# Kernel optimization log

Measured on AMD Instinct MI355X. Metric: run time of the kernel, lower is better.

## Reference

```python
import jax, jax.numpy as jnp
import numpy as np

SEQ_LEN = 1024
STRIDE = 256
FFT_LEN = 1024
B, FRAMES, BINS = 64, 512, FFT_LEN // 2 + 1


def _hann_periodic(n):
    # scipy.signal.get_window('hann', n) with fftbins=True (periodic)
    return 0.5 - 0.5 * jnp.cos(2.0 * jnp.pi * jnp.arange(n, dtype=jnp.float32) / n)


def setup_inputs() -> dict:
    key = jax.random.key(0)
    k1, k2 = jax.random.split(key)
    real = jax.random.normal(k1, (B, FRAMES, BINS), dtype=jnp.float32)
    imag = jax.random.normal(k2, (B, FRAMES, BINS), dtype=jnp.float32)
    return {"real": real, "imag": imag}


def reference(real, imag):
    # Per-frame inverse real FFT: (B, F, BINS) complex -> (B, F, FFT_LEN) real
    spec = jax.lax.complex(real, imag)
    frames = jnp.fft.irfft(spec, n=FFT_LEN, axis=-1).astype(jnp.float32)

    # Hann window, padded (symmetrically) to fft_length, then normalized by the
    # periodic overlap-added squared-window sum (Keras' COLA normalization).
    win = _hann_periodic(SEQ_LEN)
    l_pad = (FFT_LEN - SEQ_LEN) // 2
    r_pad = FFT_LEN - SEQ_LEN - l_pad
    win = jnp.pad(win, (l_pad, r_pad))
    L = SEQ_LEN + l_pad + r_pad  # == FFT_LEN here
    denom = jnp.square(win)
    overlaps = -(-L // STRIDE)  # ceil(L / stride)
    denom = jnp.pad(denom, (0, overlaps * STRIDE - L))
    denom = denom.reshape(overlaps, STRIDE).sum(0)  # periodic sum per phase
    denom = jnp.tile(denom, overlaps)[:L]
    win = jnp.where(denom > 1e-10, win / denom, 0.0)

    frames = frames * win  # (B, F, FFT_LEN)

    # Overlap-add: out[b, f*stride + n] += frames[b, f, n]
    out_len = STRIDE * (FRAMES - 1) + FFT_LEN
    idx = jnp.arange(FRAMES)[:, None] * STRIDE + jnp.arange(FFT_LEN)[None, :]  # (F, FFT_LEN)
    out = jnp.zeros((B, out_len), dtype=frames.dtype).at[:, idx].add(frames)

    # center=True trims fft_length//2 from both ends
    half = FFT_LEN // 2
    return out[:, half:out_len - half]
```

## Files before the change

kernel.cpp:

```cpp
#include <hip/hip_runtime.h>

#define BATCH    64
#define FRAMES   512
#define BINS     513
#define OUT_LEN  130816
#define HOPS_PER_BLOCK 13

__device__ __forceinline__ float2 cadd(float2 a, float2 b){ return make_float2(a.x+b.x, a.y+b.y); }
__device__ __forceinline__ float2 csub(float2 a, float2 b){ return make_float2(a.x-b.x, a.y-b.y); }
__device__ __forceinline__ float2 cmul(float2 a, float2 b){
    return make_float2(a.x*b.x - a.y*b.y, a.x*b.y + a.y*b.x);
}
__device__ __forceinline__ float2 cexp_rev(float t){
    return make_float2(__builtin_amdgcn_cosf(t), __builtin_amdgcn_sinf(t));
}
__device__ __forceinline__ int phys(int i){ return i + (i >> 4); }

__device__ __forceinline__ void bfly8(float2 v[8]) {
    float2 t0 = cadd(v[0], v[4]), t1 = csub(v[0], v[4]);
    float2 t2 = cadd(v[2], v[6]), t3 = csub(v[2], v[6]);
    float2 E0 = cadd(t0, t2), E2 = csub(t0, t2);
    float2 E1 = make_float2(t1.x - t3.y, t1.y + t3.x);
    float2 E3 = make_float2(t1.x + t3.y, t1.y - t3.x);
    float2 u0 = cadd(v[1], v[5]), u1 = csub(v[1], v[5]);
    float2 u2 = cadd(v[3], v[7]), u3 = csub(v[3], v[7]);
    float2 O0 = cadd(u0, u2), O2 = csub(u0, u2);
    float2 O1 = make_float2(u1.x - u3.y, u1.y + u3.x);
    float2 O3 = make_float2(u1.x + u3.y, u1.y - u3.x);
    const float C = 0.70710678118654752440f;
    float2 w1 = make_float2(C*(O1.x - O1.y),  C*(O1.x + O1.y));
    float2 w2 = make_float2(-O2.y, O2.x);
    float2 w3 = make_float2(-C*(O3.x + O3.y), C*(O3.x - O3.y));
    v[0] = cadd(E0, O0); v[4] = csub(E0, O0);
    v[1] = cadd(E1, w1); v[5] = csub(E1, w1);
    v[2] = cadd(E2, w2); v[6] = csub(E2, w2);
    v[3] = cadd(E3, w3); v[7] = csub(E3, w3);
}

__global__ __launch_bounds__(1024, 8) void istft_kernel(
    const float* __restrict__ re_g, const float* __restrict__ im_g,
    float* __restrict__ out)
{
    __shared__ float2 Xbuf[16][544];
    __shared__ __align__(16) float win[1024];

    const int tid  = threadIdx.x;
    const int wave = tid >> 6;
    const int lane = tid & 63;
    const int b    = blockIdx.y;
    const int u0   = blockIdx.x * HOPS_PER_BLOCK;
    const int f    = u0 - 1 + wave;
    const bool valid = (f >= 0) && (f < FRAMES);

    win[tid] = (0.5f - 0.5f * __builtin_amdgcn_cosf((float)tid * (1.0f/1024.0f)))
               * (2.0f / 3.0f / 1024.0f);

    float2* Xb = Xbuf[wave];

    if (valid) {
        const long long off = (long long)(b * FRAMES + f) * BINS;
        const float* re = re_g + off;
        const float* im = im_g + off;

        const float a0 = (float)lane * (1.0f/1024.0f);
        float2 v[8];
        #pragma unroll
        for (int j = 0; j < 8; ++j) {
            int k = lane + 64*j;
            float xar = re[k];
            float xai = (k == 0) ? 0.0f : im[k];
            float xcr = re[512 - k];
            float xci = (k == 0) ? 0.0f : im[512 - k];
            float Sx = xar + xcr, Sy = xai - xci;
            float Dx = xar - xcr, Dy = xai + xci;
            float2 tk = cexp_rev(a0 + (float)j * (1.0f/16.0f));
            v[j].x = Sx - tk.x*Dy - tk.y*Dx;
            v[j].y = Sy + tk.x*Dx - tk.y*Dy;
        }

        bfly8(v);
        {
            const float lt = (float)lane * (1.0f/512.0f);
            int basei = phys(8*lane);
            Xb[basei] = v[0];
            #pragma unroll
            for (int t = 1; t < 8; ++t)
                Xb[basei + t] = cmul(v[t], cexp_rev((float)t * lt));
        }
        {
            #pragma unroll
            for (int r = 0; r < 8; ++r) v[r] = Xb[phys(lane + 64*r)];
            bfly8(v);
            int p = lane >> 3, q = lane & 7;
            const float pf = (float)p * (1.0f/64.0f);
            Xb[phys(q + 64*p)] = v[0];
            #pragma unroll
            for (int t = 1; t < 8; ++t)
                Xb[phys(q + 64*p + 8*t)] = cmul(v[t], cexp_rev((float)t * pf));
        }
        {
            #pragma unroll
            for (int r = 0; r < 8; ++r) v[r] = Xb[phys(lane + 64*r)];
            bfly8(v);
            #pragma unroll
            for (int t = 0; t < 8; ++t) Xb[phys(lane + 64*t)] = v[t];
        }
    }
    __syncthreads();

    const int nU    = min(HOPS_PER_BLOCK, (OUT_LEN/256) - u0);
    const int nPair = nU * 128;
    float2* outp2 = (float2*)(out + (long long)b * OUT_LEN + 256 * u0);
    const float2* win2 = (const float2*)win;
    for (int pi = tid; pi < nPair; pi += 1024) {
        int o0 = pi * 2;
        int r  = o0 & 255;
        int u  = u0 + (o0 >> 8);
        float s0 = 0.0f, s1 = 0.0f;
        #pragma unroll
        for (int qq = 0; qq < 4; ++qq) {
            int ff = u + 2 - qq;
            if (ff >= 0 && ff < FRAMES) {
                int w = ff - u0 + 1;
                int h = (r >> 1) + 128*qq;
                float2 z  = Xbuf[w][phys(h)];
                float2 wn = win2[h & 511];
                s0 = fmaf(z.x, wn.x, s0);
                s1 = fmaf(z.y, wn.y, s1);
            }
        }
        outp2[pi] = make_float2(s0, s1);
    }
}

extern "C" void kernel_launch(void* const* d_in, const int* in_sizes, int n_in,
                              void* d_out, int out_size, void* d_ws, size_t ws_size,
                              hipStream_t stream) {
    const float* real = (const float*)d_in[0];
    const float* imag = (const float*)d_in[1];
    float* out = (float*)d_out;

    dim3 grid((OUT_LEN/256 + HOPS_PER_BLOCK - 1) / HOPS_PER_BLOCK, BATCH);
    dim3 block(1024);
    istft_kernel<<<grid, block, 0, stream>>>(real, imag, out);
}
```

Before: 162.5 us.

## Halve block size, each wave computes two frame FFTs, precompute twiddles

The block shrinks from 1024 to 512 threads, and each wave now runs the FFTs for two frames (A and B) in interleaved fashion, sharing per-lane twiddle factors. Twiddles come from one cexp plus complex multiplies rather than one sin/cos per element, and half the window is derived by symmetry from the same cosine. Invalid frames are zero-filled so the overlap-add loop drops its bounds checks. This raises register pressure from the two interleaved FFTs and lowers the threads available per block in exchange for more ILP and fewer transcendental calls.

```diff
diff --git a/kernel.cpp b/kernel.cpp
--- a/kernel.cpp
+++ b/kernel.cpp
@@ -37,7 +37,7 @@
     v[3] = cadd(E3, w3); v[7] = csub(E3, w3);
 }
 
-__global__ __launch_bounds__(1024, 8) void istft_kernel(
+__global__ __launch_bounds__(512, 4) void istft_kernel(
     const float* __restrict__ re_g, const float* __restrict__ im_g,
     float* __restrict__ out)
 {
@@ -49,61 +49,124 @@
     const int lane = tid & 63;
     const int b    = blockIdx.y;
     const int u0   = blockIdx.x * HOPS_PER_BLOCK;
-    const int f    = u0 - 1 + wave;
-    const bool valid = (f >= 0) && (f < FRAMES);
-
-    win[tid] = (0.5f - 0.5f * __builtin_amdgcn_cosf((float)tid * (1.0f/1024.0f)))
-               * (2.0f / 3.0f / 1024.0f);
-
-    float2* Xb = Xbuf[wave];
-
-    if (valid) {
-        const long long off = (long long)(b * FRAMES + f) * BINS;
-        const float* re = re_g + off;
-        const float* im = im_g + off;
-
-        const float a0 = (float)lane * (1.0f/1024.0f);
-        float2 v[8];
-        #pragma unroll
-        for (int j = 0; j < 8; ++j) {
-            int k = lane + 64*j;
-            float xar = re[k];
-            float xai = (k == 0) ? 0.0f : im[k];
-            float xcr = re[512 - k];
-            float xci = (k == 0) ? 0.0f : im[512 - k];
-            float Sx = xar + xcr, Sy = xai - xci;
-            float Dx = xar - xcr, Dy = xai + xci;
-            float2 tk = cexp_rev(a0 + (float)j * (1.0f/16.0f));
-            v[j].x = Sx - tk.x*Dy - tk.y*Dx;
-            v[j].y = Sy + tk.x*Dx - tk.y*Dy;
-        }
-
-        bfly8(v);
-        {
-            const float lt = (float)lane * (1.0f/512.0f);
-            int basei = phys(8*lane);
-            Xb[basei] = v[0];
-            #pragma unroll
-            for (int t = 1; t < 8; ++t)
-                Xb[basei + t] = cmul(v[t], cexp_rev((float)t * lt));
-        }
-        {
-            #pragma unroll
-            for (int r = 0; r < 8; ++r) v[r] = Xb[phys(lane + 64*r)];
-            bfly8(v);
-            int p = lane >> 3, q = lane & 7;
-            const float pf = (float)p * (1.0f/64.0f);
-            Xb[phys(q + 64*p)] = v[0];
-            #pragma unroll
-            for (int t = 1; t < 8; ++t)
-                Xb[phys(q + 64*p + 8*t)] = cmul(v[t], cexp_rev((float)t * pf));
-        }
-        {
-            #pragma unroll
-            for (int r = 0; r < 8; ++r) v[r] = Xb[phys(lane + 64*r)];
-            bfly8(v);
-            #pragma unroll
-            for (int t = 0; t < 8; ++t) Xb[phys(lane + 64*t)] = v[t];
+    const int fA   = u0 - 1 + wave;
+    const int fB   = fA + 8;
+    const bool vA  = (fA >= 0) && (fA < FRAMES);
+    const bool vB  = (fB < FRAMES);
+
+    {
+        const float K = 2.0f / 3.0f / 1024.0f;
+        float c = __builtin_amdgcn_cosf((float)tid * (1.0f/1024.0f));
+        win[tid]       = (0.5f - 0.5f*c) * K;
+        win[tid + 512] = (0.5f + 0.5f*c) * K;
+    }
+
+    float2* XA = Xbuf[wave];
+    float2* XB = Xbuf[wave + 8];
+
+    float2 tk[8];
+    tk[0] = cexp_rev((float)lane * (1.0f/1024.0f));
+    {
+        const float Cq = 0.70710678118654752440f;
+        const float Ca = 0.92387953251128675613f;
+        const float Cb = 0.38268343236508977173f;
+        const float2 C16[8] = {
+            make_float2(1.0f, 0.0f), make_float2( Ca, Cb), make_float2( Cq, Cq),
+            make_float2( Cb, Ca),    make_float2(0.0f,1.0f), make_float2(-Cb, Ca),
+            make_float2(-Cq, Cq),    make_float2(-Ca, Cb)
+        };
+        #pragma unroll
+        for (int j = 1; j < 8; ++j) tk[j] = cmul(tk[0], C16[j]);
+    }
+
+    float2 va[8], vb[8];
+    {
+        const long long offA = (long long)(b * FRAMES + fA) * BINS;
+        if (vA) {
+            const float* re = re_g + offA;
+            const float* im = im_g + offA;
+            #pragma unroll
+            for (int j = 0; j < 8; ++j) {
+                const int k = lane + 64*j;
+                float xar = re[k];
+                float xai = (k == 0) ? 0.0f : im[k];
+                float xcr = re[512 - k];
+                float xci = (k == 0) ? 0.0f : im[512 - k];
+                float Sx = xar + xcr, Sy = xai - xci;
+                float Dx = xar - xcr, Dy = xai + xci;
+                va[j].x = Sx - tk[j].x*Dy - tk[j].y*Dx;
+                va[j].y = Sy + tk[j].x*Dx - tk[j].y*Dy;
+            }
+        } else {
+            #pragma unroll
+            for (int j = 0; j < 8; ++j) va[j] = make_float2(0.0f, 0.0f);
+        }
+        if (vB) {
+            const float* re = re_g + offA + 8LL * BINS;
+            const float* im = im_g + offA + 8LL * BINS;
+            #pragma unroll
+            for (int j = 0; j < 8; ++j) {
+                const int k = lane + 64*j;
+                float xar = re[k];
+                float xai = (k == 0) ? 0.0f : im[k];
+                float xcr = re[512 - k];
+                float xci = (k == 0) ? 0.0f : im[512 - k];
+                float Sx = xar + xcr, Sy = xai - xci;
+                float Dx = xar - xcr, Dy = xai + xci;
+                vb[j].x = Sx - tk[j].x*Dy - tk[j].y*Dx;
+                vb[j].y = Sy + tk[j].x*Dx - tk[j].y*Dy;
+            }
+        } else {
+            #pragma unroll
+            for (int j = 0; j < 8; ++j) vb[j] = make_float2(0.0f, 0.0f);
+        }
+    }
+
+    bfly8(va); bfly8(vb);
+    {
+        const float2 wl = cexp_rev((float)lane * (1.0f/512.0f));
+        const int basei = phys(8*lane);
+        XA[basei] = va[0];
+        XB[basei] = vb[0];
+        float2 wt = wl;
+        #pragma unroll
+        for (int t = 1; t < 8; ++t) {
+            XA[basei + t] = cmul(va[t], wt);
+            XB[basei + t] = cmul(vb[t], wt);
+            if (t < 7) wt = cmul(wt, wl);
+        }
+    }
+    {
+        #pragma unroll
+        for (int r = 0; r < 8; ++r) {
+            va[r] = XA[phys(lane + 64*r)];
+            vb[r] = XB[phys(lane + 64*r)];
+        }
+        bfly8(va); bfly8(vb);
+        const int p = lane >> 3, q = lane & 7;
+        const float2 wp = cexp_rev((float)p * (1.0f/64.0f));
+        const int b2 = q + 64*p;
+        XA[phys(b2)] = va[0];
+        XB[phys(b2)] = vb[0];
+        float2 wt = wp;
+        #pragma unroll
+        for (int t = 1; t < 8; ++t) {
+            XA[phys(b2 + 8*t)] = cmul(va[t], wt);
+            XB[phys(b2 + 8*t)] = cmul(vb[t], wt);
+            if (t < 7) wt = cmul(wt, wp);
+        }
+    }
+    {
+        #pragma unroll
+        for (int r = 0; r < 8; ++r) {
+            va[r] = XA[phys(lane + 64*r)];
+            vb[r] = XB[phys(lane + 64*r)];
+        }
+        bfly8(va); bfly8(vb);
+        #pragma unroll
+        for (int t = 0; t < 8; ++t) {
+            XA[phys(lane + 64*t)] = va[t];
+            XB[phys(lane + 64*t)] = vb[t];
         }
     }
     __syncthreads();
@@ -112,22 +175,18 @@
     const int nPair = nU * 128;
     float2* outp2 = (float2*)(out + (long long)b * OUT_LEN + 256 * u0);
     const float2* win2 = (const float2*)win;
-    for (int pi = tid; pi < nPair; pi += 1024) {
-        int o0 = pi * 2;
-        int r  = o0 & 255;
-        int u  = u0 + (o0 >> 8);
+    for (int pi = tid; pi < nPair; pi += 512) {
+        const int h0   = pi & 127;
+        const int uoff = pi >> 7;
         float s0 = 0.0f, s1 = 0.0f;
         #pragma unroll
         for (int qq = 0; qq < 4; ++qq) {
-            int ff = u + 2 - qq;
-            if (ff >= 0 && ff < FRAMES) {
-                int w = ff - u0 + 1;
-                int h = (r >> 1) + 128*qq;
-                float2 z  = Xbuf[w][phys(h)];
-                float2 wn = win2[h & 511];
-                s0 = fmaf(z.x, wn.x, s0);
-                s1 = fmaf(z.y, wn.y, s1);
-            }
+            const int w_ = uoff + 3 - qq;
+            const int h  = h0 + 128*qq;
+            float2 z  = Xbuf[w_][phys(h)];
+            float2 wn = win2[h];
+            s0 = fmaf(z.x, wn.x, s0);
+            s1 = fmaf(z.y, wn.y, s1);
         }
         outp2[pi] = make_float2(s0, s1);
     }
@@ -141,6 +200,6 @@
     float* out = (float*)d_out;
 
     dim3 grid((OUT_LEN/256 + HOPS_PER_BLOCK - 1) / HOPS_PER_BLOCK, BATCH);
-    dim3 block(1024);
+    dim3 block(512);
     istft_kernel<<<grid, block, 0, stream>>>(real, imag, out);
 }
```

Result: no change. 164.7 us (+1.4%).
